# Performance work log

Measured on AMD Instinct MI355X. Metric: run time of the kernel, lower is better.

## Reference

```python
import jax, jax.numpy as jnp
import numpy as np
from jax import lax

L, H, DH, D, FF = 8, 16, 64, 1024, 4096  # layers, heads, head dim, model dim, mlp hidden
B, S = 4, 512
EPS = 1e-5


def setup_inputs() -> dict:
    key = jax.random.key(0)
    ks = jax.random.split(key, 8)
    std = 0.02
    return {
        "x": jax.random.normal(ks[0], (B, S, D), jnp.float32),
        "ln1_w": jnp.ones((L, D), jnp.float32),
        "ln1_b": jnp.zeros((L, D), jnp.float32),
        "qw": jax.random.normal(ks[1], (L, H, DH, DH), jnp.float32) * std,
        "qb": jnp.zeros((L, H, DH), jnp.float32),
        "kw": jax.random.normal(ks[2], (L, H, DH, DH), jnp.float32) * std,
        "kb": jnp.zeros((L, H, DH), jnp.float32),
        "vw": jax.random.normal(ks[3], (L, H, DH, DH), jnp.float32) * std,
        "vb": jnp.zeros((L, H, DH), jnp.float32),
        "ln2_w": jnp.ones((L, D), jnp.float32),
        "ln2_b": jnp.zeros((L, D), jnp.float32),
        "w1": jax.random.normal(ks[4], (L, D, FF), jnp.float32) * std,
        "b1": jnp.zeros((L, FF), jnp.float32),
        "w2": jax.random.normal(ks[5], (L, FF, D), jnp.float32) * std,
        "b2": jnp.zeros((L, D), jnp.float32),
    }


def _layernorm(x, w, b):
    m = jnp.mean(x, axis=-1, keepdims=True)
    v = jnp.mean(jnp.square(x - m), axis=-1, keepdims=True)
    return (x - m) * lax.rsqrt(v + EPS) * w + b


def reference(x, ln1_w, ln1_b, qw, qb, kw, kb, vw, vb, ln2_w, ln2_b, w1, b1, w2, b2):
    b, s, d = x.shape
    scale = 1.0 / jnp.sqrt(jnp.asarray(DH, x.dtype))

    def layer(h, p):
        (l1w, l1b, Qw, Qb, Kw, Kb, Vw, Vb, l2w, l2b, W1, B1, W2, B2) = p
        y = _layernorm(h, l1w, l1b)
        yh = y.reshape(b, s, H, DH)
        # nn.Linear per head: y @ W.T + b, W is [out=e, in=d]
        q = jnp.einsum('bshd,hed->bshe', yh, Qw) + Qb
        k = jnp.einsum('bshd,hed->bshe', yh, Kw) + Kb
        v = jnp.einsum('bshd,hed->bshe', yh, Vw) + Vb
        attn = jax.nn.softmax(jnp.einsum('bshe,bthe->bhst', q, k) * scale, axis=-1)
        o = jnp.einsum('bhst,bthe->bshe', attn, v).reshape(b, s, d)
        h = h + o
        z = _layernorm(h, l2w, l2b)
        z = jax.nn.gelu(z @ W1 + B1, approximate=False) @ W2 + B2
        return h + z, None

    params = (ln1_w, ln1_b, qw, qb, kw, kb, vw, vb, ln2_w, ln2_b, w1, b1, w2, b2)
    out, _ = lax.scan(layer, x, params)
    return out
```

## Files before the change

### kernel.cpp

```cpp
#include <hip/hip_runtime.h>
#include <hip/hip_bf16.h>

typedef __hip_bfloat16 bf16;
typedef __bf16 bf16x8 __attribute__((ext_vector_type(8)));
typedef float f32x4 __attribute__((ext_vector_type(4)));
typedef unsigned short u16;
typedef unsigned int u32;

#define SEQ 512
#define DMODEL 1024
#define FFDIM 4096
#define NHEAD 16
#define HDIM 64
#define NB 4
#define NLAYER 8

#define SBAR() asm volatile("s_barrier" ::: "memory")

__device__ __forceinline__ u16 f2bu(float f) {
    union { bf16 h; u16 u; } c; c.h = __float2bfloat16(f); return c.u;
}
__device__ __forceinline__ float bu2f(u16 u) {
    union { u32 i; float f; } c; c.i = ((u32)u) << 16; return c.f;
}

__device__ __forceinline__ void gload16(const bf16* g, bf16* l) {
    __builtin_amdgcn_global_load_lds(
        (const __attribute__((address_space(1))) unsigned int*)g,
        (__attribute__((address_space(3))) unsigned int*)l,
        16, 0, 0);
}

__device__ __forceinline__ void gemm_pipe(
    const bf16* __restrict__ A, int lda,
    const bf16* __restrict__ B, int ldb,
    int nkt,
    f32x4 (&acc)[8][2],
    char* lA, char* lB)
{
    const int tid = threadIdx.x;
    const int lane = tid & 63;
    const int wave = tid >> 6;
    const int wr = wave >> 2, wc = wave & 3;
    const int l15 = lane & 15, l4 = lane >> 4;

    auto stage = [&](int c, int t) {
        const bf16* Ak = A + t * 64;
        const bf16* Bk = B + t * 64;
        bf16* dA = (bf16*)(lA + c * 32768);
        bf16* dB = (bf16*)(lB + c * 16384);
#pragma unroll
        for (int it = 0; it < 4; ++it) {
            const int e = (it * 512 + tid) * 8;
            const int r = e >> 6;
            const int cb = (e & 63) * 2;
            const int sc = (cb ^ (((r >> 2) & 1) << 5)) >> 1;
            gload16(Ak + (long)r * lda + sc, dA + e);
        }
#pragma unroll
        for (int it = 0; it < 2; ++it) {
            const int e = (it * 512 + tid) * 8;
            const int r = e >> 6;
            const int cb = (e & 63) * 2;
            const int sc = (cb ^ (((r >> 2) & 1) << 5)) >> 1;
            gload16(Bk + (long)r * ldb + sc, dB + e);
        }
    };

    stage(0, 0);
    stage(1, 1);
    asm volatile("s_waitcnt vmcnt(6)" ::: "memory");
    SBAR();

    for (int t = 0; t < nkt; ++t) {
        const int cur = t & 1;
        const char* bA = lA + cur * 32768;
        const char* bB = lB + cur * 16384;

        bf16x8 bf_[2][2], af[8][2];
#pragma unroll
        for (int fn = 0; fn < 2; ++fn)
#pragma unroll
            for (int ks = 0; ks < 2; ++ks) {
                const int row = wc * 32 + fn * 16 + l15;
                int byte = row * 128 + (ks * 32 + l4 * 8) * 2;
                byte ^= ((row >> 2) & 1) << 5;
                bf_[fn][ks] = *(const bf16x8*)(bB + byte);
            }
#pragma unroll
        for (int i = 0; i < 8; ++i)
#pragma unroll
            for (int ks = 0; ks < 2; ++ks) {
                const int row = wr * 128 + i * 16 + l15;
                int byte = row * 128 + (ks * 32 + l4 * 8) * 2;
                byte ^= ((row >> 2) & 1) << 5;
                af[i][ks] = *(const bf16x8*)(bA + byte);
            }
        asm volatile("s_waitcnt lgkmcnt(0)" ::: "memory");
        __builtin_amdgcn_sched_barrier(0);
        SBAR();
        if (t + 2 < nkt) stage(cur, t + 2);

        __builtin_amdgcn_s_setprio(1);
#pragma unroll
        for (int i = 0; i < 8; ++i)
#pragma unroll
            for (int fn = 0; fn < 2; ++fn)
#pragma unroll
                for (int ks = 0; ks < 2; ++ks)
                    acc[i][fn] = __builtin_amdgcn_mfma_f32_16x16x32_bf16(
                        af[i][ks], bf_[fn][ks], acc[i][fn], 0, 0, 0);
        __builtin_amdgcn_s_setprio(0);

        if (t + 2 < nkt) {
            asm volatile("s_waitcnt vmcnt(6)" ::: "memory");
        } else {
            asm volatile("s_waitcnt vmcnt(0)" ::: "memory");
        }
        SBAR();
    }
}

__global__ __launch_bounds__(256) void k_ln(const float* __restrict__ h,
                                            const float* __restrict__ w,
                                            const float* __restrict__ bp,
                                            bf16* __restrict__ out,
                                            float* __restrict__ hcopy)
{
    const int row = blockIdx.x;
    const int tid = threadIdx.x;
    const float4 x = ((const float4*)(h + (long)row * DMODEL))[tid];
    if (hcopy) ((float4*)(hcopy + (long)row * DMODEL))[tid] = x;
    float s  = x.x + x.y + x.z + x.w;
    float s2 = x.x * x.x + x.y * x.y + x.z * x.z + x.w * x.w;
#pragma unroll
    for (int off = 32; off; off >>= 1) { s += __shfl_xor(s, off); s2 += __shfl_xor(s2, off); }
    __shared__ float rs[4], rs2[4];
    const int wave = tid >> 6;
    if ((tid & 63) == 0) { rs[wave] = s; rs2[wave] = s2; }
    __syncthreads();
    const float S1 = rs[0] + rs[1] + rs[2] + rs[3];
    const float S2 = rs2[0] + rs2[1] + rs2[2] + rs2[3];
    const float mean = S1 * (1.0f / DMODEL);
    const float var  = S2 * (1.0f / DMODEL) - mean * mean;
    const float rstd = rsqrtf(var + 1e-5f);
    const float4 wv = ((const float4*)w)[tid];
    const float4 bv = ((const float4*)bp)[tid];
    uint2 o;
    o.x = (u32)f2bu((x.x - mean) * rstd * wv.x + bv.x) |
          ((u32)f2bu((x.y - mean) * rstd * wv.y + bv.y) << 16);
    o.y = (u32)f2bu((x.z - mean) * rstd * wv.z + bv.z) |
          ((u32)f2bu((x.w - mean) * rstd * wv.w + bv.w) << 16);
    ((uint2*)(out + (long)row * DMODEL))[tid] = o;
}

__global__ __launch_bounds__(256) void k_transw_all(const float* __restrict__ w1,
                                                    const float* __restrict__ w2,
                                                    bf16* __restrict__ w1t,
                                                    bf16* __restrict__ w2t)
{
    int bid = blockIdx.x;
    const int l = bid >> 11;
    bid &= 2047;
    const long lofs = (long)l * DMODEL * FFDIM;
    const float* src; bf16* dst; int R, C, rb, cb;
    if (bid < 1024) {
        src = w1 + lofs; dst = w1t + lofs; R = DMODEL; C = FFDIM;
        rb = (bid >> 6) << 6; cb = (bid & 63) << 6;
    } else {
        bid -= 1024;
        src = w2 + lofs; dst = w2t + lofs; R = FFDIM; C = DMODEL;
        rb = (bid >> 4) << 6; cb = (bid & 15) << 6;
    }
    const int tid = threadIdx.x;
    const int lane = tid & 63, wave = tid >> 6;
    const int r0 = ((wave & 1) << 5) + ((lane >> 3) << 2);
    const int c0 = ((wave >> 1) << 5) + ((lane & 7) << 2);

    float4 v[4];
#pragma unroll
    for (int i = 0; i < 4; ++i)
        v[i] = *(const float4*)(src + (long)(rb + r0 + i) * C + cb + c0);
#pragma unroll
    for (int j = 0; j < 4; ++j) {
        const float a0 = (&v[0].x)[j], a1 = (&v[1].x)[j];
        const float a2 = (&v[2].x)[j], a3 = (&v[3].x)[j];
        uint2 o;
        o.x = (u32)f2bu(a0) | ((u32)f2bu(a1) << 16);
        o.y = (u32)f2bu(a2) | ((u32)f2bu(a3) << 16);
        *(uint2*)(dst + (long)(cb + c0 + j) * R + rb + r0) = o;
    }
}

__global__ __launch_bounds__(256) void k_qkv2(const bf16* __restrict__ y,
                                              const float* __restrict__ qwl,
                                              const float* __restrict__ kwl,
                                              const float* __restrict__ vwl,
                                              const float* __restrict__ qb,
                                              const float* __restrict__ kb,
                                              const float* __restrict__ vb,
                                              bf16* __restrict__ qh,
                                              bf16* __restrict__ kh,
                                              bf16* __restrict__ vt)
{
    __shared__ __align__(16) char lmem[128 * 64 * 2 + 64 * 64 * 2];
    bf16* lA = (bf16*)lmem;
    char* lBb = lmem + 128 * 64 * 2;

    const int tid = threadIdx.x;
    const int lane = tid & 63, wave = tid >> 6;
    const int l15 = lane & 15, l4 = lane >> 4;
    const int z = blockIdx.y;
    const int b = z >> 4, hd = z & 15;
    const bf16* A = y + (long)b * SEQ * DMODEL + hd * HDIM + (long)blockIdx.x * 128 * DMODEL;

#pragma unroll
    for (int it = 0; it < 4; ++it) {
        const int f = (it * 256 + tid) * 8;
        const int r = f >> 6, c = f & 63;
        gload16(A + (long)r * DMODEL + c, lA + f);
    }
    __syncthreads();

    bf16x8 qa[2][2];
#pragma unroll
    for (int fm = 0; fm < 2; ++fm)
#pragma unroll
        for (int ks = 0; ks < 2; ++ks)
            qa[fm][ks] = *(const bf16x8*)(lA + (wave * 32 + fm * 16 + l15) * 64 + ks * 32 + l4 * 8);

    for (int t = 0; t < 3; ++t) {
        __syncthreads();
        const float* Bsrc = ((t == 0) ? qwl : (t == 1) ? kwl : vwl) + (long)hd * HDIM * HDIM;
#pragma unroll
        for (int it = 0; it < 4; ++it) {
            const int f = (it * 256 + tid) * 4;
            const float4 v = *(const float4*)(Bsrc + f);
            uint2 o;
            o.x = (u32)f2bu(v.x) | ((u32)f2bu(v.y) << 16);
            o.y = (u32)f2bu(v.z) | ((u32)f2bu(v.w) << 16);
            const int row = f >> 6;
            const int byte = (f << 1) ^ ((row & 7) << 4);
            *(uint2*)(lBb + byte) = o;
        }
        __syncthreads();

        bf16x8 bfr[4][2];
#pragma unroll
        for (int fn = 0; fn < 4; ++fn)
#pragma unroll
            for (int ks = 0; ks < 2; ++ks) {
                const int row = fn * 16 + l15;
                int byte = (row << 7) + ((ks * 32 + l4 * 8) << 1);
                byte ^= (row & 7) << 4;
                bfr[fn][ks] = *(const bf16x8*)(lBb + byte);
            }
        f32x4 acc[2][4] = {};
#pragma unroll
        for (int ks = 0; ks < 2; ++ks)
#pragma unroll
            for (int fm = 0; fm < 2; ++fm)
#pragma unroll
                for (int fn = 0; fn < 4; ++fn)
                    acc[fm][fn] = __builtin_amdgcn_mfma_f32_16x16x32_bf16(
                        qa[fm][ks], bfr[fn][ks], acc[fm][fn], 0, 0, 0);

        const float* bias = (t == 0) ? qb : (t == 1) ? kb : vb;
#pragma unroll
        for (int fm = 0; fm < 2; ++fm)
#pragma unroll
            for (int fn = 0; fn < 4; ++fn)
#pragma unroll
                for (int r = 0; r < 4; ++r) {
                    const int srow = blockIdx.x * 128 + wave * 32 + fm * 16 + l4 * 4 + r;
                    const int e = fn * 16 + l15;
                    float v = acc[fm][fn][r] + bias[hd * HDIM + e];
                    if (t == 0) {
                        qh[((long)z * SEQ + srow) * HDIM + e] = __float2bfloat16(v * 0.125f);
                    } else if (t == 1) {
                        kh[((long)z * SEQ + srow) * HDIM + e] = __float2bfloat16(v);
                    } else {
                        vt[((long)z * HDIM + e) * SEQ + srow] = __float2bfloat16(v);
                    }
                }
    }
}

__global__ __launch_bounds__(256) void k_flash(const bf16* __restrict__ qh,
                                               const bf16* __restrict__ kh,
                                               const bf16* __restrict__ vt,
                                               float* __restrict__ h)
{
    __shared__ __align__(16) char lmem[24576];
    bf16* lQ = (bf16*)lmem;
    char* lKb = lmem + 8192;
    char* lVb = lmem + 16384;

    const int tid = threadIdx.x;
    const int lane = tid & 63, wave = tid >> 6;
    const int l15 = lane & 15, l4 = lane >> 4;
    const int z = blockIdx.y;
    const int b = z >> 4, hd = z & 15;
    const int q0 = blockIdx.x * 64;

    const bf16* Qsrc = qh + ((long)z * SEQ + q0) * HDIM;
#pragma unroll
    for (int it = 0; it < 2; ++it) {
        const int f = (it * 256 + tid) * 8;
        gload16(Qsrc + f, lQ + f);
    }
    __syncthreads();

    bf16x8 qa[2];
#pragma unroll
    for (int ks = 0; ks < 2; ++ks)
        qa[ks] = *(const bf16x8*)(lQ + (wave * 16 + l15) * 64 + ks * 32 + l4 * 8);

    char* lPb = lmem + wave * 2048;

    f32x4 O[4] = {};
    float mrun[4], lrun[4];
#pragma unroll
    for (int r = 0; r < 4; ++r) { mrun[r] = -1e30f; lrun[r] = 0.0f; }

    for (int kv = 0; kv < SEQ / 64; ++kv) {
        __syncthreads();
        const bf16* Ksrc = kh + ((long)z * SEQ + kv * 64) * HDIM;
#pragma unroll
        for (int it = 0; it < 2; ++it) {
            const int f = (it * 256 + tid) * 8;
            const int r = f >> 6;
            const uint4 v = *(const uint4*)(Ksrc + f);
            *(uint4*)(lKb + ((f << 1) ^ ((r & 7) << 4))) = v;
        }
        const bf16* Vsrc = vt + (long)z * HDIM * SEQ + kv * 64;
#pragma unroll
        for (int it = 0; it < 2; ++it) {
            const int f = (it * 256 + tid) * 8;
            const int r = f >> 6, c = f & 63;
            const uint4 v = *(const uint4*)(Vsrc + (long)r * SEQ + c);
            *(uint4*)(lVb + ((f << 1) ^ ((r & 7) << 4))) = v;
        }
        __syncthreads();

        f32x4 sa[4];
#pragma unroll
        for (int fn = 0; fn < 4; ++fn) sa[fn] = (f32x4){0.f, 0.f, 0.f, 0.f};
#pragma unroll
        for (int ks = 0; ks < 2; ++ks)
#pragma unroll
            for (int fn = 0; fn < 4; ++fn) {
                const int row = fn * 16 + l15;
                int byte = (row << 7) + ((ks * 32 + l4 * 8) << 1);
                byte ^= (row & 7) << 4;
                const bf16x8 kb_ = *(const bf16x8*)(lKb + byte);
                sa[fn] = __builtin_amdgcn_mfma_f32_16x16x32_bf16(qa[ks], kb_, sa[fn], 0, 0, 0);
            }

#pragma unroll
        for (int r = 0; r < 4; ++r) {
            float mx = fmaxf(fmaxf(sa[0][r], sa[1][r]), fmaxf(sa[2][r], sa[3][r]));
#pragma unroll
            for (int m_ = 1; m_ < 16; m_ <<= 1) mx = fmaxf(mx, __shfl_xor(mx, m_));
            const float nm = fmaxf(mrun[r], mx);
            const float al = __expf(mrun[r] - nm);
            mrun[r] = nm;
            float p0 = __expf(sa[0][r] - nm), p1 = __expf(sa[1][r] - nm);
            float p2 = __expf(sa[2][r] - nm), p3 = __expf(sa[3][r] - nm);
            float ps = p0 + p1 + p2 + p3;
#pragma unroll
            for (int m_ = 1; m_ < 16; m_ <<= 1) ps += __shfl_xor(ps, m_);
            lrun[r] = lrun[r] * al + ps;
#pragma unroll
            for (int fn = 0; fn < 4; ++fn) O[fn][r] *= al;
            const int row = l4 * 4 + r;
            const int rsw = (row & 7) << 4;
            const int rb = row << 7;
            *(u16*)(lPb + ((rb + ((0 * 16 + l15) << 1)) ^ rsw)) = f2bu(p0);
            *(u16*)(lPb + ((rb + ((1 * 16 + l15) << 1)) ^ rsw)) = f2bu(p1);
            *(u16*)(lPb + ((rb + ((2 * 16 + l15) << 1)) ^ rsw)) = f2bu(p2);
            *(u16*)(lPb + ((rb + ((3 * 16 + l15) << 1)) ^ rsw)) = f2bu(p3);
        }

#pragma unroll
        for (int ks = 0; ks < 2; ++ks) {
            const int rowp = l15;
            int pbyte = (rowp << 7) + ((ks * 32 + l4 * 8) << 1);
            pbyte ^= (rowp & 7) << 4;
            const bf16x8 pa = *(const bf16x8*)(lPb + pbyte);
#pragma unroll
            for (int fn = 0; fn < 4; ++fn) {
                const int row = fn * 16 + l15;
                int byte = (row << 7) + ((ks * 32 + l4 * 8) << 1);
                byte ^= (row & 7) << 4;
                const bf16x8 vb_ = *(const bf16x8*)(lVb + byte);
                O[fn] = __builtin_amdgcn_mfma_f32_16x16x32_bf16(pa, vb_, O[fn], 0, 0, 0);
            }
        }
    }

    float rinv[4];
#pragma unroll
    for (int r = 0; r < 4; ++r) rinv[r] = 1.0f / lrun[r];
#pragma unroll
    for (int fn = 0; fn < 4; ++fn)
#pragma unroll
        for (int r = 0; r < 4; ++r) {
            const int srow = q0 + wave * 16 + l4 * 4 + r;
            const int e = fn * 16 + l15;
            h[((long)b * SEQ + srow) * DMODEL + hd * HDIM + e] += O[fn][r] * rinv[r];
        }
}

__global__ __launch_bounds__(512, 2) void k_gemm1(const bf16* __restrict__ zb,
                                                  const bf16* __restrict__ w1t,
                                                  const float* __restrict__ b1,
                                                  bf16* __restrict__ ff1)
{
    __shared__ __align__(16) char lmem[98304];
    const int bx = (int)blockIdx.y >> 2;
    const int by = (int)blockIdx.x * 4 + ((int)blockIdx.y & 3);
    const bf16* A = zb + (long)bx * 256 * DMODEL;
    const bf16* B = w1t + (long)by * 128 * DMODEL;
    f32x4 acc[8][2] = {};
    gemm_pipe(A, DMODEL, B, DMODEL, DMODEL / 64, acc, lmem, lmem + 65536);

    const int lane = threadIdx.x & 63, wave = threadIdx.x >> 6;
    const int wr = wave >> 2, wc = wave & 3;
    const int l15 = lane & 15, l4 = lane >> 4;
#pragma unroll
    for (int fm = 0; fm < 8; ++fm)
#pragma unroll
        for (int fn = 0; fn < 2; ++fn)
#pragma unroll
            for (int r = 0; r < 4; ++r) {
                const int row = bx * 256 + wr * 128 + fm * 16 + l4 * 4 + r;
                const int col = by * 128 + wc * 32 + fn * 16 + l15;
                const float x = acc[fm][fn][r] + b1[col];
                const float g = 0.5f * x * (1.0f + erff(x * 0.70710678118f));
                ff1[(long)row * FFDIM + col] = __float2bfloat16(g);
            }
}

__global__ __launch_bounds__(512, 2) void k_gemm2(const bf16* __restrict__ ff1,
                                                  const bf16* __restrict__ w2t,
                                                  bf16* __restrict__ part)
{
    __shared__ __align__(16) char lmem[98304];
    const int sk = blockIdx.z;
    const int bx = (int)blockIdx.y;
    const int by = (int)blockIdx.x;
    const bf16* A = ff1 + (long)bx * 256 * FFDIM + (long)sk * 1024;
    const bf16* B = w2t + (long)by * 128 * FFDIM + (long)sk * 1024;
    f32x4 acc[8][2] = {};
    gemm_pipe(A, FFDIM, B, FFDIM, 1024 / 64, acc, lmem, lmem + 65536);

    bf16* out = part + (long)sk * (NB * SEQ) * DMODEL;
    const int lane = threadIdx.x & 63, wave = threadIdx.x >> 6;
    const int wr = wave >> 2, wc = wave & 3;
    const int l15 = lane & 15, l4 = lane >> 4;
#pragma unroll
    for (int fm = 0; fm < 8; ++fm)
#pragma unroll
        for (int fn = 0; fn < 2; ++fn)
#pragma unroll
            for (int r = 0; r < 4; ++r) {
                const int row = bx * 256 + wr * 128 + fm * 16 + l4 * 4 + r;
                const int col = by * 128 + wc * 32 + fn * 16 + l15;
                out[(long)row * DMODEL + col] = __float2bfloat16(acc[fm][fn][r]);
            }
}

__global__ __launch_bounds__(256) void k_red2ln(const bf16* __restrict__ part,
                                                const float* __restrict__ b2,
                                                float* __restrict__ h,
                                                const float* __restrict__ lnw,
                                                const float* __restrict__ lnb,
                                                bf16* __restrict__ y,
                                                int do_ln)
{
    constexpr long NELT = (long)NB * SEQ * DMODEL;
    const long row = blockIdx.x;
    const int tid = threadIdx.x;
    const long e0 = row * DMODEL + tid * 4;
    float sum[4] = {0.f, 0.f, 0.f, 0.f};
#pragma unroll
    for (int sk = 0; sk < 4; ++sk) {
        const uint2 u = *(const uint2*)(part + sk * NELT + e0);
        sum[0] += bu2f((u16)(u.x & 0xffffu));
        sum[1] += bu2f((u16)(u.x >> 16));
        sum[2] += bu2f((u16)(u.y & 0xffffu));
        sum[3] += bu2f((u16)(u.y >> 16));
    }
    const float4 bv = ((const float4*)b2)[tid];
    float4 hv = ((float4*)h)[row * (DMODEL / 4) + tid];
    hv.x += sum[0] + bv.x;
    hv.y += sum[1] + bv.y;
    hv.z += sum[2] + bv.z;
    hv.w += sum[3] + bv.w;
    ((float4*)h)[row * (DMODEL / 4) + tid] = hv;

    if (!do_ln) return;
    float ss  = hv.x + hv.y + hv.z + hv.w;
    float ss2 = hv.x * hv.x + hv.y * hv.y + hv.z * hv.z + hv.w * hv.w;
#pragma unroll
    for (int off = 32; off; off >>= 1) { ss += __shfl_xor(ss, off); ss2 += __shfl_xor(ss2, off); }
    __shared__ float rs[4], rs2[4];
    const int wave = tid >> 6;
    if ((tid & 63) == 0) { rs[wave] = ss; rs2[wave] = ss2; }
    __syncthreads();
    const float S1 = rs[0] + rs[1] + rs[2] + rs[3];
    const float S2 = rs2[0] + rs2[1] + rs2[2] + rs2[3];
    const float mean = S1 * (1.0f / DMODEL);
    const float var  = S2 * (1.0f / DMODEL) - mean * mean;
    const float rstd = rsqrtf(var + 1e-5f);
    const float4 wv = ((const float4*)lnw)[tid];
    const float4 lb = ((const float4*)lnb)[tid];
    uint2 o;
    o.x = (u32)f2bu((hv.x - mean) * rstd * wv.x + lb.x) |
          ((u32)f2bu((hv.y - mean) * rstd * wv.y + lb.y) << 16);
    o.y = (u32)f2bu((hv.z - mean) * rstd * wv.z + lb.z) |
          ((u32)f2bu((hv.w - mean) * rstd * wv.w + lb.w) << 16);
    ((uint2*)(y + row * DMODEL))[tid] = o;
}

extern "C" void kernel_launch(void* const* d_in, const int* in_sizes, int n_in,
                              void* d_out, int out_size, void* d_ws, size_t ws_size,
                              hipStream_t stream)
{
    const float* x    = (const float*)d_in[0];
    const float* ln1w = (const float*)d_in[1];
    const float* ln1b = (const float*)d_in[2];
    const float* qw   = (const float*)d_in[3];
    const float* qb   = (const float*)d_in[4];
    const float* kw   = (const float*)d_in[5];
    const float* kb   = (const float*)d_in[6];
    const float* vw   = (const float*)d_in[7];
    const float* vb   = (const float*)d_in[8];
    const float* ln2w = (const float*)d_in[9];
    const float* ln2b = (const float*)d_in[10];
    const float* w1   = (const float*)d_in[11];
    const float* b1   = (const float*)d_in[12];
    const float* w2   = (const float*)d_in[13];
    const float* b2   = (const float*)d_in[14];

    char* ws = (char*)d_ws;
    const size_t MB = 1024 * 1024;
    bf16* y    = (bf16*)(ws + 0 * MB);
    bf16* zb   = (bf16*)(ws + 4 * MB);
    bf16* qh   = (bf16*)(ws + 8 * MB);
    bf16* kh   = (bf16*)(ws + 12 * MB);
    bf16* vt   = (bf16*)(ws + 16 * MB);
    bf16* ff1  = (bf16*)(ws + 20 * MB);
    bf16* part = (bf16*)(ws + 36 * MB);
    bf16* w1tA = (bf16*)(ws + 68 * MB);
    bf16* w2tA = (bf16*)(ws + 132 * MB);

    float* h = (float*)d_out;

    k_transw_all<<<NLAYER * 2048, 256, 0, stream>>>(w1, w2, w1tA, w2tA);
    k_ln<<<NB * SEQ, 256, 0, stream>>>(x, ln1w, ln1b, y, h);

    for (int l = 0; l < NLAYER; ++l) {
        const long wofs = (long)l * DMODEL * FFDIM;
        k_qkv2<<<dim3(4, NB * NHEAD), 256, 0, stream>>>(
            y, qw + (long)l * 65536, kw + (long)l * 65536, vw + (long)l * 65536,
            qb + l * NHEAD * HDIM, kb + l * NHEAD * HDIM, vb + l * NHEAD * HDIM,
            qh, kh, vt);
        k_flash<<<dim3(SEQ / 64, NB * NHEAD), 256, 0, stream>>>(qh, kh, vt, h);
        k_ln<<<NB * SEQ, 256, 0, stream>>>(h, ln2w + l * DMODEL, ln2b + l * DMODEL, zb,
                                           nullptr);
        k_gemm1<<<dim3(8, 32), 512, 0, stream>>>(zb, w1tA + wofs, b1 + l * FFDIM, ff1);
        k_gemm2<<<dim3(8, 8, 4), 512, 0, stream>>>(ff1, w2tA + wofs, part);
        const int last = (l == NLAYER - 1);
        k_red2ln<<<NB * SEQ, 256, 0, stream>>>(part, b2 + l * DMODEL, h,
                                               ln1w + (l + 1) * DMODEL * (1 - last),
                                               ln1b + (l + 1) * DMODEL * (1 - last),
                                               y, !last);
    }
}
```

Measured before the change: 992.3 us.

## Pre-tile weights into contiguous swizzled blocks and interleave A-fragment loads with MFMAs

The weight conversion kernel now writes W1/W2 as contiguous pre-swizzled 128x64 bf16 tiles, using an LDS transpose, so each GEMM stage loads its B tile with linear 16-byte copies instead of strided, swizzled row reads. The GEMM inner loop also now loads A fragments in four chunks interleaved with the MFMAs, instead of loading all of them before a full lgkmcnt wait. The next-stage prefetch is moved after the compute. This aims to cut address math and improve B-load coalescing, and to overlap LDS reads with matrix ops, at the cost of a later prefetch issue and a changed weight layout that every consumer must match.

Result: faster. 926.6 us (-6.6%).

```diff
diff --git a/kernel.cpp b/kernel.cpp
--- a/kernel.cpp
+++ b/kernel.cpp
@@ -33,7 +33,7 @@
 
 __device__ __forceinline__ void gemm_pipe(
     const bf16* __restrict__ A, int lda,
-    const bf16* __restrict__ B, int ldb,
+    const bf16* __restrict__ Bt,
     int nkt,
     f32x4 (&acc)[8][2],
     char* lA, char* lB)
@@ -46,7 +46,6 @@
 
     auto stage = [&](int c, int t) {
         const bf16* Ak = A + t * 64;
-        const bf16* Bk = B + t * 64;
         bf16* dA = (bf16*)(lA + c * 32768);
         bf16* dB = (bf16*)(lB + c * 16384);
 #pragma unroll
@@ -57,13 +56,11 @@
             const int sc = (cb ^ (((r >> 2) & 1) << 5)) >> 1;
             gload16(Ak + (long)r * lda + sc, dA + e);
         }
+        const bf16* Bk = Bt + (long)t * 8192;
 #pragma unroll
         for (int it = 0; it < 2; ++it) {
             const int e = (it * 512 + tid) * 8;
-            const int r = e >> 6;
-            const int cb = (e & 63) * 2;
-            const int sc = (cb ^ (((r >> 2) & 1) << 5)) >> 1;
-            gload16(Bk + (long)r * ldb + sc, dB + e);
+            gload16(Bk + e, dB + e);
         }
     };
 
@@ -77,7 +74,7 @@
         const char* bA = lA + cur * 32768;
         const char* bB = lB + cur * 16384;
 
-        bf16x8 bf_[2][2], af[8][2];
+        bf16x8 bf_[2][2];
 #pragma unroll
         for (int fn = 0; fn < 2; ++fn)
 #pragma unroll
@@ -88,31 +85,31 @@
                 bf_[fn][ks] = *(const bf16x8*)(bB + byte);
             }
 #pragma unroll
-        for (int i = 0; i < 8; ++i)
-#pragma unroll
-            for (int ks = 0; ks < 2; ++ks) {
-                const int row = wr * 128 + i * 16 + l15;
-                int byte = row * 128 + (ks * 32 + l4 * 8) * 2;
-                byte ^= ((row >> 2) & 1) << 5;
-                af[i][ks] = *(const bf16x8*)(bA + byte);
-            }
-        asm volatile("s_waitcnt lgkmcnt(0)" ::: "memory");
-        __builtin_amdgcn_sched_barrier(0);
+        for (int q = 0; q < 4; ++q) {
+            bf16x8 af[2][2];
+#pragma unroll
+            for (int i = 0; i < 2; ++i)
+#pragma unroll
+                for (int ks = 0; ks < 2; ++ks) {
+                    const int row = wr * 128 + (q * 2 + i) * 16 + l15;
+                    int byte = row * 128 + (ks * 32 + l4 * 8) * 2;
+                    byte ^= ((row >> 2) & 1) << 5;
+                    af[i][ks] = *(const bf16x8*)(bA + byte);
+                }
+            __builtin_amdgcn_s_setprio(1);
+#pragma unroll
+            for (int i = 0; i < 2; ++i)
+#pragma unroll
+                for (int fn = 0; fn < 2; ++fn)
+#pragma unroll
+                    for (int ks = 0; ks < 2; ++ks)
+                        acc[q * 2 + i][fn] = __builtin_amdgcn_mfma_f32_16x16x32_bf16(
+                            af[i][ks], bf_[fn][ks], acc[q * 2 + i][fn], 0, 0, 0);
+            __builtin_amdgcn_s_setprio(0);
+        }
         SBAR();
-        if (t + 2 < nkt) stage(cur, t + 2);
-
-        __builtin_amdgcn_s_setprio(1);
-#pragma unroll
-        for (int i = 0; i < 8; ++i)
-#pragma unroll
-            for (int fn = 0; fn < 2; ++fn)
-#pragma unroll
-                for (int ks = 0; ks < 2; ++ks)
-                    acc[i][fn] = __builtin_amdgcn_mfma_f32_16x16x32_bf16(
-                        af[i][ks], bf_[fn][ks], acc[i][fn], 0, 0, 0);
-        __builtin_amdgcn_s_setprio(0);
-
         if (t + 2 < nkt) {
+            stage(cur, t + 2);
             asm volatile("s_waitcnt vmcnt(6)" ::: "memory");
         } else {
             asm volatile("s_waitcnt vmcnt(0)" ::: "memory");
@@ -154,41 +151,57 @@
     ((uint2*)(out + (long)row * DMODEL))[tid] = o;
 }
 
-__global__ __launch_bounds__(256) void k_transw_all(const float* __restrict__ w1,
-                                                    const float* __restrict__ w2,
-                                                    bf16* __restrict__ w1t,
-                                                    bf16* __restrict__ w2t)
-{
+__global__ __launch_bounds__(256) void k_tilew(const float* __restrict__ w1,
+                                               const float* __restrict__ w2,
+                                               bf16* __restrict__ w1t,
+                                               bf16* __restrict__ w2t)
+{
+    __shared__ u16 t[64][138];
     int bid = blockIdx.x;
-    const int l = bid >> 11;
-    bid &= 2047;
+    const int l = bid >> 10;
+    bid &= 1023;
     const long lofs = (long)l * DMODEL * FFDIM;
-    const float* src; bf16* dst; int R, C, rb, cb;
-    if (bid < 1024) {
-        src = w1 + lofs; dst = w1t + lofs; R = DMODEL; C = FFDIM;
-        rb = (bid >> 6) << 6; cb = (bid & 63) << 6;
+    const float* src; bf16* dst; int ldsrc;
+    if (bid < 512) {
+        const int by = bid >> 4, kt = bid & 15;
+        src = w1 + lofs + (long)(kt * 64) * FFDIM + by * 128;
+        ldsrc = FFDIM;
+        dst = w1t + lofs + ((long)by * 16 + kt) * 8192;
     } else {
-        bid -= 1024;
-        src = w2 + lofs; dst = w2t + lofs; R = FFDIM; C = DMODEL;
-        rb = (bid >> 4) << 6; cb = (bid & 15) << 6;
+        bid -= 512;
+        const int by = bid >> 6, kt = bid & 63;
+        src = w2 + lofs + (long)(kt * 64) * DMODEL + by * 128;
+        ldsrc = DMODEL;
+        dst = w2t + lofs + ((long)by * 64 + kt) * 8192;
     }
     const int tid = threadIdx.x;
-    const int lane = tid & 63, wave = tid >> 6;
-    const int r0 = ((wave & 1) << 5) + ((lane >> 3) << 2);
-    const int c0 = ((wave >> 1) << 5) + ((lane & 7) << 2);
-
-    float4 v[4];
-#pragma unroll
-    for (int i = 0; i < 4; ++i)
-        v[i] = *(const float4*)(src + (long)(rb + r0 + i) * C + cb + c0);
-#pragma unroll
-    for (int j = 0; j < 4; ++j) {
-        const float a0 = (&v[0].x)[j], a1 = (&v[1].x)[j];
-        const float a2 = (&v[2].x)[j], a3 = (&v[3].x)[j];
-        uint2 o;
-        o.x = (u32)f2bu(a0) | ((u32)f2bu(a1) << 16);
-        o.y = (u32)f2bu(a2) | ((u32)f2bu(a3) << 16);
-        *(uint2*)(dst + (long)(cb + c0 + j) * R + rb + r0) = o;
+    const int n4 = (tid & 31) * 4;
+    const int kr = tid >> 5;
+#pragma unroll
+    for (int j = 0; j < 8; ++j) {
+        const int k = j * 8 + kr;
+        const float4 v = *(const float4*)(src + (long)k * ldsrc + n4);
+        t[k][n4]     = f2bu(v.x);
+        t[k][n4 + 1] = f2bu(v.y);
+        t[k][n4 + 2] = f2bu(v.z);
+        t[k][n4 + 3] = f2bu(v.w);
+    }
+    __syncthreads();
+#pragma unroll
+    for (int it = 0; it < 4; ++it) {
+        const int e0 = it * 2048 + tid * 8;
+        const int r = e0 >> 6;
+        const int c = e0 & 63;
+        const int ksw = c ^ (((r >> 2) & 1) << 4);
+        u16 v[8];
+#pragma unroll
+        for (int m = 0; m < 8; ++m) v[m] = t[ksw + m][r];
+        uint4 o;
+        o.x = (u32)v[0] | ((u32)v[1] << 16);
+        o.y = (u32)v[2] | ((u32)v[3] << 16);
+        o.z = (u32)v[4] | ((u32)v[5] << 16);
+        o.w = (u32)v[6] | ((u32)v[7] << 16);
+        *(uint4*)(dst + e0) = o;
     }
 }
 
@@ -421,9 +434,9 @@
     const int bx = (int)blockIdx.y >> 2;
     const int by = (int)blockIdx.x * 4 + ((int)blockIdx.y & 3);
     const bf16* A = zb + (long)bx * 256 * DMODEL;
-    const bf16* B = w1t + (long)by * 128 * DMODEL;
+    const bf16* Bt = w1t + (long)by * 16 * 8192;
     f32x4 acc[8][2] = {};
-    gemm_pipe(A, DMODEL, B, DMODEL, DMODEL / 64, acc, lmem, lmem + 65536);
+    gemm_pipe(A, DMODEL, Bt, DMODEL / 64, acc, lmem, lmem + 65536);
 
     const int lane = threadIdx.x & 63, wave = threadIdx.x >> 6;
     const int wr = wave >> 2, wc = wave & 3;
@@ -451,9 +464,9 @@
     const int bx = (int)blockIdx.y;
     const int by = (int)blockIdx.x;
     const bf16* A = ff1 + (long)bx * 256 * FFDIM + (long)sk * 1024;
-    const bf16* B = w2t + (long)by * 128 * FFDIM + (long)sk * 1024;
+    const bf16* Bt = w2t + ((long)by * 64 + sk * 16) * 8192;
     f32x4 acc[8][2] = {};
-    gemm_pipe(A, FFDIM, B, FFDIM, 1024 / 64, acc, lmem, lmem + 65536);
+    gemm_pipe(A, FFDIM, Bt, 1024 / 64, acc, lmem, lmem + 65536);
 
     bf16* out = part + (long)sk * (NB * SEQ) * DMODEL;
     const int lane = threadIdx.x & 63, wave = threadIdx.x >> 6;
@@ -558,7 +571,7 @@
 
     float* h = (float*)d_out;
 
-    k_transw_all<<<NLAYER * 2048, 256, 0, stream>>>(w1, w2, w1tA, w2tA);
+    k_tilew<<<NLAYER * 1024, 256, 0, stream>>>(w1, w2, w1tA, w2tA);
     k_ln<<<NB * SEQ, 256, 0, stream>>>(x, ln1w, ln1b, y, h);
 
     for (int l = 0; l < NLAYER; ++l) {
```
